# Kernel optimization log

Measured on AMD Instinct MI355X. Metric: run time of the kernel, lower is better.

Reference implementation:

```python
import jax, jax.numpy as jnp
import numpy as np

K = 7
G = 16
PAD = K // 2
EPS = 1e-5


def setup_inputs() -> dict:
    key = jax.random.key(0)
    ks = jax.random.split(key, 8)
    C = 256
    Cr = C // 4  # ratio=4 bottleneck
    inputs = jax.random.normal(ks[0], (4, C, 56, 56), dtype=jnp.float32)
    W1 = jax.random.normal(ks[1], (Cr, C), dtype=jnp.float32) * 0.05
    b1 = jax.random.normal(ks[2], (Cr,), dtype=jnp.float32) * 0.05
    gamma = jax.random.normal(ks[3], (Cr,), dtype=jnp.float32) * 0.1 + 1.0
    beta = jax.random.normal(ks[4], (Cr,), dtype=jnp.float32) * 0.1
    mean = jax.random.normal(ks[5], (Cr,), dtype=jnp.float32) * 0.1
    var = jax.random.uniform(ks[6], (Cr,), dtype=jnp.float32) * 0.5 + 0.5
    W2 = jax.random.normal(ks[7], (G * K * K, Cr), dtype=jnp.float32) * 0.05
    b2 = jnp.zeros((G * K * K,), dtype=jnp.float32)
    return {"inputs": inputs, "W1": W1, "b1": b1, "gamma": gamma,
            "beta": beta, "mean": mean, "var": var, "W2": W2, "b2": b2}


def reference(inputs, W1, b1, gamma, beta, mean, var, W2, b2):
    B, C, H, W = inputs.shape
    Cg = C // G
    # kernel-generation branch: 1x1 conv -> BN (eval stats) -> relu -> 1x1 conv
    t = jnp.einsum('bchw,oc->bohw', inputs, W1) + b1[None, :, None, None]
    scale = gamma / jnp.sqrt(var + EPS)
    t = t * scale[None, :, None, None] + (beta - mean * scale)[None, :, None, None]
    t = jax.nn.relu(t)
    w = jnp.einsum('bchw,oc->bohw', t, W2) + b2[None, :, None, None]
    w = w.reshape(B, G, K * K, H, W)  # per-pixel kernel
    # involution: accumulate shifted slices instead of materializing unfold
    xp = jnp.pad(inputs, ((0, 0), (0, 0), (PAD, PAD), (PAD, PAD)))
    xg = xp.reshape(B, G, Cg, H + 2 * PAD, W + 2 * PAD)
    out = jnp.zeros((B, G, Cg, H, W), dtype=inputs.dtype)
    k = 0
    for i in range(K):
        for j in range(K):
            out = out + xg[:, :, :, i:i + H, j:j + W] * w[:, :, k][:, :, None, :, :]
            k += 1
    return out.reshape(B, C, H, W)
```

## Files before the change

### kernel.cpp

```cpp
#include <hip/hip_runtime.h>

#define HW    3136
#define HDIM  56
#define CIN   256
#define CR    64
#define NG    16
#define KK    49
#define BEPS  1e-5f
#define RB    2
#define NBAND 28
#define WSTR  116
#define XROWS 8
#define XSTR  68

typedef __attribute__((ext_vector_type(8))) short short8;
typedef __attribute__((ext_vector_type(4))) float f32x4;

__device__ __forceinline__ unsigned short f2bf(float f) {
    union { float f; unsigned u; } v; v.f = f;
    unsigned r = (v.u + 0x7FFFu + ((v.u >> 16) & 1u)) >> 16;
    return (unsigned short)r;
}

__global__ __launch_bounds__(256) void k0_prep(
    const float* __restrict__ W1, const float* __restrict__ b1,
    const float* __restrict__ gamma, const float* __restrict__ beta,
    const float* __restrict__ mean, const float* __restrict__ var,
    const float* __restrict__ W2,
    unsigned short* __restrict__ W1b, unsigned short* __restrict__ W2bT,
    float* __restrict__ b1f)
{
    int idx = blockIdx.x * 256 + threadIdx.x;
    if (idx < CR * CIN) {
        int o = idx >> 8;
        float s = gamma[o] * rsqrtf(var[o] + BEPS);
        W1b[idx] = f2bf(W1[idx] * s);
    } else if (idx < CR * CIN + NG * 64 * 64) {
        int j = idx - CR * CIN;
        int c = j & 63, tap = (j >> 6) & 63, g = j >> 12;
        float v = (tap < KK) ? W2[(g * KK + tap) * CR + c] : 0.f;
        W2bT[j] = f2bf(v);
    } else if (idx < CR * CIN + NG * 64 * 64 + CR) {
        int o = idx - CR * CIN - NG * 64 * 64;
        float s = gamma[o] * rsqrtf(var[o] + BEPS);
        b1f[o] = b1[o] * s + beta[o] - mean[o] * s;
    }
}

__global__ __launch_bounds__(256) void k1_gemm(
    const float* __restrict__ x, const unsigned short* __restrict__ W1b,
    const float* __restrict__ b1f, unsigned short* __restrict__ t_bf)
{
    const int tid = threadIdx.x;
    const int b = blockIdx.y;
    const int lane = tid & 63, l15 = lane & 15, q = lane >> 4;
    const int wid = tid >> 6;
    const int pxb = blockIdx.x * 64 + wid * 16;

    const float* xp = x + (size_t)b * CIN * HW + pxb + l15;

    f32x4 acc[4];
#pragma unroll
    for (int nt = 0; nt < 4; nt++) acc[nt] = (f32x4){0.f, 0.f, 0.f, 0.f};

#pragma unroll 2
    for (int kc = 0; kc < 8; kc++) {
        short8 af;
#pragma unroll
        for (int j = 0; j < 8; j++) {
            float xv = xp[(size_t)(kc * 32 + q * 8 + j) * HW];
            af[j] = (short)f2bf(xv);
        }
#pragma unroll
        for (int nt = 0; nt < 4; nt++) {
            short8 bf = *(const short8*)&W1b[(size_t)(16 * nt + l15) * CIN + kc * 32 + q * 8];
            acc[nt] = __builtin_amdgcn_mfma_f32_16x16x32_bf16(af, bf, acc[nt], 0, 0, 0);
        }
    }
#pragma unroll
    for (int nt = 0; nt < 4; nt++) {
        float bias = b1f[16 * nt + l15];
#pragma unroll
        for (int r = 0; r < 4; r++) {
            int px = pxb + 4 * q + r;
            float v = fmaxf(acc[nt][r] + bias, 0.f);
            t_bf[((size_t)b * HW + px) * CR + 16 * nt + l15] = f2bf(v);
        }
    }
}

__global__ __launch_bounds__(256, 4) void k2_fused(
    const float* __restrict__ x, const unsigned short* __restrict__ t_bf,
    const unsigned short* __restrict__ W2bT, const float* __restrict__ b2,
    float* __restrict__ out)
{
    __shared__ float w_lds[KK * WSTR];
    __shared__ float x_lds[XROWS * 8 * XSTR];

    const int tid = threadIdx.x;
    const int band = blockIdx.x, g = blockIdx.y;
    const int b = blockIdx.z >> 1, half = blockIdx.z & 1;
    const int h0 = band * RB;
    const int lane = tid & 63, l15 = lane & 15, q = lane >> 4;
    const int wid = tid >> 6;

    for (int i = tid; i < XROWS * 8 * XSTR; i += 256) {
        int col = i % XSTR; int t2 = i / XSTR; int cg = t2 & 7; int rowx = t2 >> 3;
        int hy = h0 - 3 + rowx, xc = col - 4;
        float v = 0.f;
        if (hy >= 0 && hy < HDIM && xc >= 0 && xc < HDIM)
            v = x[((size_t)b * CIN + g * 16 + half * 8 + cg) * HW + hy * HDIM + xc];
        x_lds[i] = v;
    }

    {
        short8 bfr[4][2];
#pragma unroll
        for (int nt = 0; nt < 4; nt++)
#pragma unroll
            for (int ks = 0; ks < 2; ks++)
                bfr[nt][ks] = *(const short8*)&W2bT[((size_t)g * 64 + 16 * nt + l15) * 64 + ks * 32 + q * 8];
        float b2v[4];
#pragma unroll
        for (int nt = 0; nt < 4; nt++) {
            int tap = 16 * nt + l15;
            b2v[nt] = (tap < KK) ? b2[g * KK + tap] : 0.f;
        }
        for (int mt = wid; mt < 7; mt += 4) {
            const unsigned short* tp = &t_bf[((size_t)b * HW + h0 * HDIM + mt * 16 + l15) * CR];
            short8 a0 = *(const short8*)&tp[q * 8];
            short8 a1 = *(const short8*)&tp[32 + q * 8];
#pragma unroll
            for (int nt = 0; nt < 4; nt++) {
                f32x4 acc = (f32x4){0.f, 0.f, 0.f, 0.f};
                acc = __builtin_amdgcn_mfma_f32_16x16x32_bf16(a0, bfr[nt][0], acc, 0, 0, 0);
                acc = __builtin_amdgcn_mfma_f32_16x16x32_bf16(a1, bfr[nt][1], acc, 0, 0, 0);
                int tap = 16 * nt + l15;
                if (tap < KK) {
                    *(float4*)&w_lds[tap * WSTR + mt * 16 + 4 * q] =
                        make_float4(acc[0] + b2v[nt], acc[1] + b2v[nt],
                                    acc[2] + b2v[nt], acc[3] + b2v[nt]);
                }
            }
        }
    }
    __syncthreads();

    if (tid < 224) {
        const int quad = tid >> 4;
        const int rem  = tid & 15;
        const int row  = rem >> 3;
        const int cg   = rem & 7;
        const int colb = quad * 4, h = h0 + row;

        float acc[4] = {0.f, 0.f, 0.f, 0.f};

#pragma unroll
        for (int di = 0; di < 7; di++) {
            float wv[7][4];
#pragma unroll
            for (int dj = 0; dj < 7; dj++) {
                float4 wq = *(const float4*)&w_lds[(di * 7 + dj) * WSTR + row * HDIM + colb];
                wv[dj][0] = wq.x; wv[dj][1] = wq.y; wv[dj][2] = wq.z; wv[dj][3] = wq.w;
            }
            const float* xr = &x_lds[((row + di) * 8 + cg) * XSTR + colb];
            float4 A  = *(const float4*)&xr[0];
            float4 Bv = *(const float4*)&xr[4];
            float4 Cv = *(const float4*)&xr[8];
            float win[12] = {A.x, A.y, A.z, A.w, Bv.x, Bv.y, Bv.z, Bv.w,
                             Cv.x, Cv.y, Cv.z, Cv.w};
#pragma unroll
            for (int dj = 0; dj < 7; dj++)
#pragma unroll
                for (int kk = 0; kk < 4; kk++)
                    acc[kk] += win[kk + dj + 1] * wv[dj][kk];
        }
        float* op = &out[((size_t)b * CIN + g * 16 + half * 8 + cg) * HW + h * HDIM + colb];
        *(float4*)op = make_float4(acc[0], acc[1], acc[2], acc[3]);
    }
}

extern "C" void kernel_launch(void* const* d_in, const int* in_sizes, int n_in,
                              void* d_out, int out_size, void* d_ws, size_t ws_size,
                              hipStream_t stream) {
    const float* x     = (const float*)d_in[0];
    const float* W1    = (const float*)d_in[1];
    const float* b1    = (const float*)d_in[2];
    const float* gamma = (const float*)d_in[3];
    const float* beta  = (const float*)d_in[4];
    const float* mean  = (const float*)d_in[5];
    const float* var   = (const float*)d_in[6];
    const float* W2    = (const float*)d_in[7];
    const float* b2    = (const float*)d_in[8];
    float* out = (float*)d_out;

    unsigned short* t_bf = (unsigned short*)d_ws;
    unsigned short* W1b  = t_bf + (size_t)4 * HW * CR;
    unsigned short* W2bT = W1b + CR * CIN;
    float* b1f           = (float*)(W2bT + NG * 64 * 64);

    int n_k0 = CR * CIN + NG * 64 * 64 + CR;
    k0_prep<<<(n_k0 + 255) / 256, 256, 0, stream>>>(
        W1, b1, gamma, beta, mean, var, W2, W1b, W2bT, b1f);

    dim3 g1(HW / 64, 4);
    k1_gemm<<<g1, 256, 0, stream>>>(x, W1b, b1f, t_bf);

    dim3 g2(NBAND, NG, 8);
    k2_fused<<<g2, 256, 0, stream>>>(x, t_bf, W2bT, b2, out);
}
```

Measured before the change: 133.7 us.

## Process all 16 group channels per block to reuse generated kernel weights

Each k2 block now handles all 16 channels of a group instead of splitting them into two halves, so the per-pixel kernel weights (the W2 MFMA and the w_lds fill) are computed once per band instead of twice. Each thread accumulates two channels and reuses the loaded weight registers across them. The grid is halved, the x tile in LDS doubles, and launch bounds drop to 2 blocks per SM. This trades occupancy and parallelism for less redundant GEMM work and fewer LDS weight reads.

```diff
diff --git a/kernel.cpp b/kernel.cpp
--- a/kernel.cpp
+++ b/kernel.cpp
@@ -11,7 +11,7 @@
 #define NBAND 28
 #define WSTR  116
 #define XROWS 8
-#define XSTR  68
+#define XCGS  72
 
 typedef __attribute__((ext_vector_type(8))) short short8;
 typedef __attribute__((ext_vector_type(4))) float f32x4;
@@ -89,27 +89,26 @@
     }
 }
 
-__global__ __launch_bounds__(256, 4) void k2_fused(
+__global__ __launch_bounds__(256, 2) void k2_fused(
     const float* __restrict__ x, const unsigned short* __restrict__ t_bf,
     const unsigned short* __restrict__ W2bT, const float* __restrict__ b2,
     float* __restrict__ out)
 {
     __shared__ float w_lds[KK * WSTR];
-    __shared__ float x_lds[XROWS * 8 * XSTR];
+    __shared__ float x_lds[XROWS * 16 * XCGS];
 
     const int tid = threadIdx.x;
-    const int band = blockIdx.x, g = blockIdx.y;
-    const int b = blockIdx.z >> 1, half = blockIdx.z & 1;
+    const int band = blockIdx.x, g = blockIdx.y, b = blockIdx.z;
     const int h0 = band * RB;
     const int lane = tid & 63, l15 = lane & 15, q = lane >> 4;
     const int wid = tid >> 6;
 
-    for (int i = tid; i < XROWS * 8 * XSTR; i += 256) {
-        int col = i % XSTR; int t2 = i / XSTR; int cg = t2 & 7; int rowx = t2 >> 3;
+    for (int i = tid; i < XROWS * 16 * XCGS; i += 256) {
+        int col = i % XCGS; int t2 = i / XCGS; int cg = t2 & 15; int rowx = t2 >> 4;
         int hy = h0 - 3 + rowx, xc = col - 4;
         float v = 0.f;
         if (hy >= 0 && hy < HDIM && xc >= 0 && xc < HDIM)
-            v = x[((size_t)b * CIN + g * 16 + half * 8 + cg) * HW + hy * HDIM + xc];
+            v = x[((size_t)b * CIN + g * 16 + cg) * HW + hy * HDIM + xc];
         x_lds[i] = v;
     }
 
@@ -150,10 +149,14 @@
         const int quad = tid >> 4;
         const int rem  = tid & 15;
         const int row  = rem >> 3;
-        const int cg   = rem & 7;
+        const int cgp  = rem & 7;
         const int colb = quad * 4, h = h0 + row;
 
-        float acc[4] = {0.f, 0.f, 0.f, 0.f};
+        float acc[2][4];
+#pragma unroll
+        for (int i = 0; i < 2; i++)
+#pragma unroll
+            for (int k = 0; k < 4; k++) acc[i][k] = 0.f;
 
 #pragma unroll
         for (int di = 0; di < 7; di++) {
@@ -163,20 +166,26 @@
                 float4 wq = *(const float4*)&w_lds[(di * 7 + dj) * WSTR + row * HDIM + colb];
                 wv[dj][0] = wq.x; wv[dj][1] = wq.y; wv[dj][2] = wq.z; wv[dj][3] = wq.w;
             }
-            const float* xr = &x_lds[((row + di) * 8 + cg) * XSTR + colb];
-            float4 A  = *(const float4*)&xr[0];
-            float4 Bv = *(const float4*)&xr[4];
-            float4 Cv = *(const float4*)&xr[8];
-            float win[12] = {A.x, A.y, A.z, A.w, Bv.x, Bv.y, Bv.z, Bv.w,
-                             Cv.x, Cv.y, Cv.z, Cv.w};
-#pragma unroll
-            for (int dj = 0; dj < 7; dj++)
-#pragma unroll
-                for (int kk = 0; kk < 4; kk++)
-                    acc[kk] += win[kk + dj + 1] * wv[dj][kk];
-        }
-        float* op = &out[((size_t)b * CIN + g * 16 + half * 8 + cg) * HW + h * HDIM + colb];
-        *(float4*)op = make_float4(acc[0], acc[1], acc[2], acc[3]);
+#pragma unroll
+            for (int cgi = 0; cgi < 2; cgi++) {
+                const float* xr = &x_lds[((row + di) * 16 + cgp + cgi * 8) * XCGS + colb];
+                float4 A  = *(const float4*)&xr[0];
+                float4 Bv = *(const float4*)&xr[4];
+                float4 Cv = *(const float4*)&xr[8];
+                float win[12] = {A.x, A.y, A.z, A.w, Bv.x, Bv.y, Bv.z, Bv.w,
+                                 Cv.x, Cv.y, Cv.z, Cv.w};
+#pragma unroll
+                for (int dj = 0; dj < 7; dj++)
+#pragma unroll
+                    for (int kk = 0; kk < 4; kk++)
+                        acc[cgi][kk] += win[kk + dj + 1] * wv[dj][kk];
+            }
+        }
+#pragma unroll
+        for (int cgi = 0; cgi < 2; cgi++) {
+            float* op = &out[((size_t)b * CIN + g * 16 + cgp + cgi * 8) * HW + h * HDIM + colb];
+            *(float4*)op = make_float4(acc[cgi][0], acc[cgi][1], acc[cgi][2], acc[cgi][3]);
+        }
     }
 }
 
@@ -206,6 +215,6 @@
     dim3 g1(HW / 64, 4);
     k1_gemm<<<g1, 256, 0, stream>>>(x, W1b, b1f, t_bf);
 
-    dim3 g2(NBAND, NG, 8);
+    dim3 g2(NBAND, NG, 4);
     k2_fused<<<g2, 256, 0, stream>>>(x, t_bf, W2bT, b2, out);
 }
```

Measured after the change: 155.0 us. +15.9%, slower.

## Read involution input straight from global memory and reshape launch grids

Applied to the files above, without the earlier changes.

The x tile staging in LDS is removed from the fused involution kernel; each thread now loads its 3 float4 window segments per kernel row directly from global memory, with masks for padding. Occupancy hint rises to 8 blocks per CU since LDS usage drops, and the grid order puts group/half fastest so neighbouring blocks share the same band and batch, which may help L2 reuse of t_bf and x. The GEMM kernel is split into single-wave blocks over 16 pixels each. The trade is redundant global/L2 traffic for the overlapping x windows in exchange for no LDS fill and no extra sync work.

```diff
diff --git a/kernel.cpp b/kernel.cpp
--- a/kernel.cpp
+++ b/kernel.cpp
@@ -10,8 +10,6 @@
 #define RB    2
 #define NBAND 28
 #define WSTR  116
-#define XROWS 8
-#define XSTR  68
 
 typedef __attribute__((ext_vector_type(8))) short short8;
 typedef __attribute__((ext_vector_type(4))) float f32x4;
@@ -47,15 +45,13 @@
     }
 }
 
-__global__ __launch_bounds__(256) void k1_gemm(
+__global__ __launch_bounds__(64) void k1_gemm(
     const float* __restrict__ x, const unsigned short* __restrict__ W1b,
     const float* __restrict__ b1f, unsigned short* __restrict__ t_bf)
 {
-    const int tid = threadIdx.x;
+    const int lane = threadIdx.x & 63, l15 = lane & 15, q = lane >> 4;
     const int b = blockIdx.y;
-    const int lane = tid & 63, l15 = lane & 15, q = lane >> 4;
-    const int wid = tid >> 6;
-    const int pxb = blockIdx.x * 64 + wid * 16;
+    const int pxb = blockIdx.x * 16;
 
     const float* xp = x + (size_t)b * CIN * HW + pxb + l15;
 
@@ -89,29 +85,19 @@
     }
 }
 
-__global__ __launch_bounds__(256, 4) void k2_fused(
+__global__ __launch_bounds__(256, 8) void k2_fused(
     const float* __restrict__ x, const unsigned short* __restrict__ t_bf,
     const unsigned short* __restrict__ W2bT, const float* __restrict__ b2,
     float* __restrict__ out)
 {
     __shared__ float w_lds[KK * WSTR];
-    __shared__ float x_lds[XROWS * 8 * XSTR];
 
     const int tid = threadIdx.x;
-    const int band = blockIdx.x, g = blockIdx.y;
-    const int b = blockIdx.z >> 1, half = blockIdx.z & 1;
+    const int g = blockIdx.x >> 1, half = blockIdx.x & 1;
+    const int band = blockIdx.y, b = blockIdx.z;
     const int h0 = band * RB;
     const int lane = tid & 63, l15 = lane & 15, q = lane >> 4;
     const int wid = tid >> 6;
-
-    for (int i = tid; i < XROWS * 8 * XSTR; i += 256) {
-        int col = i % XSTR; int t2 = i / XSTR; int cg = t2 & 7; int rowx = t2 >> 3;
-        int hy = h0 - 3 + rowx, xc = col - 4;
-        float v = 0.f;
-        if (hy >= 0 && hy < HDIM && xc >= 0 && xc < HDIM)
-            v = x[((size_t)b * CIN + g * 16 + half * 8 + cg) * HW + hy * HDIM + xc];
-        x_lds[i] = v;
-    }
 
     {
         short8 bfr[4][2];
@@ -151,24 +137,34 @@
         const int rem  = tid & 15;
         const int row  = rem >> 3;
         const int cg   = rem & 7;
-        const int colb = quad * 4, h = h0 + row;
-
+        const int colb = quad * 4;
+        const int cb   = colb - 4;
+        const int h    = h0 + row;
+        const bool okL = quad > 0, okR = quad < 13;
+
+        const float* xch = x + ((size_t)b * CIN + g * 16 + half * 8 + cg) * HW;
+        const float4 z4 = make_float4(0.f, 0.f, 0.f, 0.f);
         float acc[4] = {0.f, 0.f, 0.f, 0.f};
 
 #pragma unroll
         for (int di = 0; di < 7; di++) {
+            int hy = h + di - 3;
+            bool rok = (hy >= 0) & (hy < HDIM);
+            int hyc = min(max(hy, 0), HDIM - 1);
+            const float* xrow = xch + hyc * HDIM;
+
+            float4 A  = (rok && okL) ? *(const float4*)&xrow[cb]     : z4;
+            float4 Bv = rok          ? *(const float4*)&xrow[cb + 4] : z4;
+            float4 Cv = (rok && okR) ? *(const float4*)&xrow[cb + 8] : z4;
+            float win[12] = {A.x, A.y, A.z, A.w, Bv.x, Bv.y, Bv.z, Bv.w,
+                             Cv.x, Cv.y, Cv.z, Cv.w};
+
             float wv[7][4];
 #pragma unroll
             for (int dj = 0; dj < 7; dj++) {
                 float4 wq = *(const float4*)&w_lds[(di * 7 + dj) * WSTR + row * HDIM + colb];
                 wv[dj][0] = wq.x; wv[dj][1] = wq.y; wv[dj][2] = wq.z; wv[dj][3] = wq.w;
             }
-            const float* xr = &x_lds[((row + di) * 8 + cg) * XSTR + colb];
-            float4 A  = *(const float4*)&xr[0];
-            float4 Bv = *(const float4*)&xr[4];
-            float4 Cv = *(const float4*)&xr[8];
-            float win[12] = {A.x, A.y, A.z, A.w, Bv.x, Bv.y, Bv.z, Bv.w,
-                             Cv.x, Cv.y, Cv.z, Cv.w};
 #pragma unroll
             for (int dj = 0; dj < 7; dj++)
 #pragma unroll
@@ -203,9 +199,9 @@
     k0_prep<<<(n_k0 + 255) / 256, 256, 0, stream>>>(
         W1, b1, gamma, beta, mean, var, W2, W1b, W2bT, b1f);
 
-    dim3 g1(HW / 64, 4);
-    k1_gemm<<<g1, 256, 0, stream>>>(x, W1b, b1f, t_bf);
-
-    dim3 g2(NBAND, NG, 8);
+    dim3 g1(HW / 16, 4);
+    k1_gemm<<<g1, 64, 0, stream>>>(x, W1b, b1f, t_bf);
+
+    dim3 g2(NG * 2, NBAND, 4);
     k2_fused<<<g2, 256, 0, stream>>>(x, t_bf, W2bT, b2, out);
 }
```

Measured after the change: 174.8 us. 1.31x slower.

## Split kernel generation from involution via global per-pixel weights buffer

Applied to the files above, without the earlier changes.

The fused kernel-generation plus involution kernel is split in two. One kernel computes per-pixel 49-tap weights with MFMA and writes them to a workspace buffer in global memory. A second kernel reads those weights directly from global memory during the involution, which removes the duplicated MFMA work that the two channel halves each did. The first GEMM kernel moves to 64-thread blocks, and the fused path's occupancy hint drops to 2. The split costs about 39 MB of extra global writes and reads, and it falls back to the fused kernel when the workspace is too small.

```diff
diff --git a/kernel.cpp b/kernel.cpp
--- a/kernel.cpp
+++ b/kernel.cpp
@@ -10,7 +10,6 @@
 #define RB    2
 #define NBAND 28
 #define WSTR  116
-#define XROWS 8
 #define XSTR  68
 
 typedef __attribute__((ext_vector_type(8))) short short8;
@@ -47,15 +46,13 @@
     }
 }
 
-__global__ __launch_bounds__(256) void k1_gemm(
+__global__ __launch_bounds__(64) void k1_gemm(
     const float* __restrict__ x, const unsigned short* __restrict__ W1b,
     const float* __restrict__ b1f, unsigned short* __restrict__ t_bf)
 {
-    const int tid = threadIdx.x;
+    const int lane = threadIdx.x & 63, l15 = lane & 15, q = lane >> 4;
     const int b = blockIdx.y;
-    const int lane = tid & 63, l15 = lane & 15, q = lane >> 4;
-    const int wid = tid >> 6;
-    const int pxb = blockIdx.x * 64 + wid * 16;
+    const int pxb = blockIdx.x * 16;
 
     const float* xp = x + (size_t)b * CIN * HW + pxb + l15;
 
@@ -89,13 +86,111 @@
     }
 }
 
-__global__ __launch_bounds__(256, 4) void k2_fused(
+__global__ __launch_bounds__(256) void k2a_kgen(
+    const unsigned short* __restrict__ t_bf, const unsigned short* __restrict__ W2bT,
+    const float* __restrict__ b2, float* __restrict__ w_g)
+{
+    const int tid = threadIdx.x;
+    const int lane = tid & 63, l15 = lane & 15, q = lane >> 4;
+    const int wid = tid >> 6;
+    const int g = blockIdx.y, b = blockIdx.z;
+    const int pxb = blockIdx.x * 64 + wid * 16;
+
+    short8 bfr[4][2];
+#pragma unroll
+    for (int nt = 0; nt < 4; nt++)
+#pragma unroll
+        for (int ks = 0; ks < 2; ks++)
+            bfr[nt][ks] = *(const short8*)&W2bT[((size_t)g * 64 + 16 * nt + l15) * 64 + ks * 32 + q * 8];
+    float b2v[4];
+#pragma unroll
+    for (int nt = 0; nt < 4; nt++) {
+        int tap = 16 * nt + l15;
+        b2v[nt] = (tap < KK) ? b2[g * KK + tap] : 0.f;
+    }
+
+    const unsigned short* tp = &t_bf[((size_t)b * HW + pxb + l15) * CR];
+    short8 a0 = *(const short8*)&tp[q * 8];
+    short8 a1 = *(const short8*)&tp[32 + q * 8];
+
+#pragma unroll
+    for (int nt = 0; nt < 4; nt++) {
+        f32x4 acc = (f32x4){0.f, 0.f, 0.f, 0.f};
+        acc = __builtin_amdgcn_mfma_f32_16x16x32_bf16(a0, bfr[nt][0], acc, 0, 0, 0);
+        acc = __builtin_amdgcn_mfma_f32_16x16x32_bf16(a1, bfr[nt][1], acc, 0, 0, 0);
+        int tap = 16 * nt + l15;
+        if (tap < KK) {
+            *(float4*)&w_g[(((size_t)b * NG + g) * KK + tap) * HW + pxb + 4 * q] =
+                make_float4(acc[0] + b2v[nt], acc[1] + b2v[nt],
+                            acc[2] + b2v[nt], acc[3] + b2v[nt]);
+        }
+    }
+}
+
+__global__ __launch_bounds__(256) void k2b_inv(
+    const float* __restrict__ x, const float* __restrict__ w_g,
+    float* __restrict__ out)
+{
+    __shared__ float x_lds[8 * 8 * XSTR];
+
+    const int tid = threadIdx.x;
+    const int band = blockIdx.x;
+    const int g = blockIdx.y >> 1, half = blockIdx.y & 1;
+    const int b = blockIdx.z;
+    const int h0 = band * RB;
+
+    for (int i = tid; i < 8 * 8 * XSTR; i += 256) {
+        int col = i % XSTR; int t2 = i / XSTR; int cg = t2 & 7; int rowx = t2 >> 3;
+        int hy = h0 - 3 + rowx, xc = col - 4;
+        float v = 0.f;
+        if (hy >= 0 && hy < HDIM && xc >= 0 && xc < HDIM)
+            v = x[((size_t)b * CIN + g * 16 + half * 8 + cg) * HW + hy * HDIM + xc];
+        x_lds[i] = v;
+    }
+    __syncthreads();
+
+    if (tid < 224) {
+        const int quad = tid >> 4;
+        const int rem  = tid & 15;
+        const int row  = rem >> 3;
+        const int cg   = rem & 7;
+        const int colb = quad * 4, h = h0 + row;
+
+        const float* wg = &w_g[(((size_t)b * NG + g) * KK) * HW + h * HDIM + colb];
+        float acc[4] = {0.f, 0.f, 0.f, 0.f};
+
+#pragma unroll
+        for (int di = 0; di < 7; di++) {
+            float wv[7][4];
+#pragma unroll
+            for (int dj = 0; dj < 7; dj++) {
+                float4 wq = *(const float4*)&wg[(size_t)(di * 7 + dj) * HW];
+                wv[dj][0] = wq.x; wv[dj][1] = wq.y; wv[dj][2] = wq.z; wv[dj][3] = wq.w;
+            }
+            const float* xr = &x_lds[((row + di) * 8 + cg) * XSTR + colb];
+            float4 A  = *(const float4*)&xr[0];
+            float4 Bv = *(const float4*)&xr[4];
+            float4 Cv = *(const float4*)&xr[8];
+            float win[12] = {A.x, A.y, A.z, A.w, Bv.x, Bv.y, Bv.z, Bv.w,
+                             Cv.x, Cv.y, Cv.z, Cv.w};
+#pragma unroll
+            for (int dj = 0; dj < 7; dj++)
+#pragma unroll
+                for (int kk = 0; kk < 4; kk++)
+                    acc[kk] += win[kk + dj + 1] * wv[dj][kk];
+        }
+        float* op = &out[((size_t)b * CIN + g * 16 + half * 8 + cg) * HW + h * HDIM + colb];
+        *(float4*)op = make_float4(acc[0], acc[1], acc[2], acc[3]);
+    }
+}
+
+__global__ __launch_bounds__(256, 2) void k2_fused(
     const float* __restrict__ x, const unsigned short* __restrict__ t_bf,
     const unsigned short* __restrict__ W2bT, const float* __restrict__ b2,
     float* __restrict__ out)
 {
     __shared__ float w_lds[KK * WSTR];
-    __shared__ float x_lds[XROWS * 8 * XSTR];
+    __shared__ float x_lds[8 * 8 * XSTR];
 
     const int tid = threadIdx.x;
     const int band = blockIdx.x, g = blockIdx.y;
@@ -104,7 +199,7 @@
     const int lane = tid & 63, l15 = lane & 15, q = lane >> 4;
     const int wid = tid >> 6;
 
-    for (int i = tid; i < XROWS * 8 * XSTR; i += 256) {
+    for (int i = tid; i < 8 * 8 * XSTR; i += 256) {
         int col = i % XSTR; int t2 = i / XSTR; int cg = t2 & 7; int rowx = t2 >> 3;
         int hy = h0 - 3 + rowx, xc = col - 4;
         float v = 0.f;
@@ -112,7 +207,6 @@
             v = x[((size_t)b * CIN + g * 16 + half * 8 + cg) * HW + hy * HDIM + xc];
         x_lds[i] = v;
     }
-
     {
         short8 bfr[4][2];
 #pragma unroll
@@ -154,7 +248,6 @@
         const int colb = quad * 4, h = h0 + row;
 
         float acc[4] = {0.f, 0.f, 0.f, 0.f};
-
 #pragma unroll
         for (int di = 0; di < 7; di++) {
             float wv[7][4];
@@ -194,18 +287,36 @@
     const float* b2    = (const float*)d_in[8];
     float* out = (float*)d_out;
 
-    unsigned short* t_bf = (unsigned short*)d_ws;
+    const size_t n_wg = (size_t)4 * NG * KK * HW;
+    float* w_g           = (float*)d_ws;
+    unsigned short* t_bf = (unsigned short*)(w_g + n_wg);
     unsigned short* W1b  = t_bf + (size_t)4 * HW * CR;
     unsigned short* W2bT = W1b + CR * CIN;
     float* b1f           = (float*)(W2bT + NG * 64 * 64);
+    const size_t needed  = n_wg * 4 + (802816 + 16384 + 65536) * 2 + 64 * 4;
+
+    bool split = ws_size >= needed;
+    if (!split) {
+        t_bf = (unsigned short*)d_ws;
+        W1b  = t_bf + (size_t)4 * HW * CR;
+        W2bT = W1b + CR * CIN;
+        b1f  = (float*)(W2bT + NG * 64 * 64);
+    }
 
     int n_k0 = CR * CIN + NG * 64 * 64 + CR;
     k0_prep<<<(n_k0 + 255) / 256, 256, 0, stream>>>(
         W1, b1, gamma, beta, mean, var, W2, W1b, W2bT, b1f);
 
-    dim3 g1(HW / 64, 4);
-    k1_gemm<<<g1, 256, 0, stream>>>(x, W1b, b1f, t_bf);
-
-    dim3 g2(NBAND, NG, 8);
-    k2_fused<<<g2, 256, 0, stream>>>(x, t_bf, W2bT, b2, out);
-}
+    dim3 g1(HW / 16, 4);
+    k1_gemm<<<g1, 64, 0, stream>>>(x, W1b, b1f, t_bf);
+
+    if (split) {
+        dim3 ga(HW / 64, NG, 4);
+        k2a_kgen<<<ga, 256, 0, stream>>>(t_bf, W2bT, b2, w_g);
+        dim3 gb(NBAND, NG * 2, 4);
+        k2b_inv<<<gb, 256, 0, stream>>>(x, w_g, out);
+    } else {
+        dim3 g2(NBAND, NG, 8);
+        k2_fused<<<g2, 256, 0, stream>>>(x, t_bf, W2bT, b2, out);
+    }
+}
```

Result: slower. 140.2 us (+4.9%).
